# Optimization experiments

Measured on AMD Instinct MI355X. Metric: run time of the kernel, lower is better.

The kernel has to match this reference:

```python
import jax, jax.numpy as jnp
import numpy as np

# Fixed module configuration (matches init_kwargs)
B, T, H, W, C = 2, 16, 32, 32, 512
NH, DH = 8, 64          # num_heads, head_dim = C // NH
MLP = 2048
EPS = 1e-6              # flax LayerNorm default epsilon


def _xavier(key, shape):
    fan_in, fan_out = shape[-2], shape[-1]
    lim = np.sqrt(6.0 / (fan_in + fan_out)).astype(np.float32)
    return jax.random.uniform(key, shape, jnp.float32, -lim, lim)


def setup_inputs() -> dict:
    key = jax.random.key(0)
    ks = jax.random.split(key, 8)
    return {
        "x": jax.random.normal(ks[0], (B, T * H * W, C), jnp.float32),
        # per-axis (stacked: 0=time, 1=height, 2=width) attention params
        "ln_scale": jnp.ones((3, C), jnp.float32),
        "ln_bias": jnp.zeros((3, C), jnp.float32),
        "wq": _xavier(ks[1], (3, C, C)), "bq": jnp.zeros((3, C), jnp.float32),
        "wk": _xavier(ks[2], (3, C, C)), "bk": jnp.zeros((3, C), jnp.float32),
        "wv": _xavier(ks[3], (3, C, C)), "bv": jnp.zeros((3, C), jnp.float32),
        "wo": _xavier(ks[4], (3, C, C)), "bo": jnp.zeros((3, C), jnp.float32),
        # final LN + MLP params
        "ln_mlp_scale": jnp.ones((C,), jnp.float32),
        "ln_mlp_bias": jnp.zeros((C,), jnp.float32),
        "w1": _xavier(ks[5], (C, MLP)),
        "b1": jax.random.normal(ks[6], (MLP,), jnp.float32) * 1e-6,
        "w2": _xavier(ks[7], (MLP, C)),
        "b2": jnp.zeros((C,), jnp.float32),
    }


def _ln(x, scale, bias):
    m = jnp.mean(x, axis=-1, keepdims=True)
    v = jnp.var(x, axis=-1, keepdims=True)
    return (x - m) * jax.lax.rsqrt(v + EPS) * scale + bias


def _mha(x, wq, bq, wk, bk, wv, bv, wo, bo):
    # x: [Bf, S, C]; standard flax-style MHA (query scaled by 1/sqrt(head_dim))
    Bf, S, _ = x.shape
    q = (x @ wq + bq).reshape(Bf, S, NH, DH) * (1.0 / np.sqrt(DH).astype(np.float32))
    k = (x @ wk + bk).reshape(Bf, S, NH, DH)
    v = (x @ wv + bv).reshape(Bf, S, NH, DH)
    a = jax.nn.softmax(jnp.einsum('bqhd,bkhd->bhqk', q, k), axis=-1)
    o = jnp.einsum('bhqk,bkhd->bqhd', a, v).reshape(Bf, S, C)
    return o @ wo + bo


def _axial(x5, axis, sc, bi, wq, bq, wk, bk, wv, bv, wo, bo):
    # fold all non-`axis` spatial dims into batch, attend along `axis`
    other = [a for a in (1, 2, 3) if a != axis]
    perm = [0] + other + [axis, 4]
    xp = jnp.transpose(x5, perm)                      # [..., S_axis, C]
    pshape = xp.shape
    x1 = xp.reshape(-1, pshape[-2], C)                # [Bf, S_axis, C]
    y = _mha(_ln(x1, sc, bi), wq, bq, wk, bk, wv, bv, wo, bo) + x1  # pre-LN residual
    y = y.reshape(pshape)
    inv = list(np.argsort(perm))
    return jnp.transpose(y, inv)


def reference(x, ln_scale, ln_bias, wq, bq, wk, bk, wv, bv, wo, bo,
              ln_mlp_scale, ln_mlp_bias, w1, b1, w2, b2):
    x5 = x.reshape(B, T, H, W, C)
    for i, axis in enumerate((1, 2, 3)):  # time, height, width
        x5 = _axial(x5, axis, ln_scale[i], ln_bias[i], wq[i], bq[i],
                    wk[i], bk[i], wv[i], bv[i], wo[i], bo[i])
    xf = x5.reshape(B, T * H * W, C)
    y = _ln(xf, ln_mlp_scale, ln_mlp_bias)
    y = jax.nn.gelu(y @ w1 + b1) @ w2 + b2            # gelu approximate=True (flax default)
    return xf + y
```

## Files before the change

kernel.cpp:

```cpp
#include <hip/hip_runtime.h>
#include <hip/hip_bf16.h>

typedef __attribute__((ext_vector_type(8))) short short8;
typedef __attribute__((ext_vector_type(4))) float f32x4;

static __device__ __forceinline__ short f2bf(float f) {
    union { __hip_bfloat16 h; short s; } u;
    u.h = __float2bfloat16(f);
    return u.s;
}

static __device__ __forceinline__ float gelu_tanh(float v) {
    const float c = 0.7978845608028654f;
    float t = tanhf(c * (v + 0.044715f * v * v * v));
    return 0.5f * v * (1.f + t);
}

static __device__ __forceinline__ void gload16(const void* g, void* l) {
    __builtin_amdgcn_global_load_lds(
        (const __attribute__((address_space(1))) void*)g,
        (__attribute__((address_space(3))) void*)l, 16, 0, 0);
}

__global__ __launch_bounds__(256) void cvt_weights(
    const float* __restrict__ wq, const float* __restrict__ wk,
    const float* __restrict__ wv, const float* __restrict__ wo,
    const float* __restrict__ w1, const float* __restrict__ w2,
    short* __restrict__ wT)
{
    const long NSQ = 12L * 262144;
    long gid = (long)blockIdx.x * 256 + threadIdx.x;
    if (gid < NSQ) {
        int m = (int)(gid >> 18);
        int rem = (int)(gid & 262143);
        int n = rem >> 9, k = rem & 511;
        int a = m >> 2, t = m & 3;
        const float* src = (t == 0) ? wq : (t == 1) ? wk : (t == 2) ? wv : wo;
        wT[gid] = f2bf(src[(long)a * 262144 + (long)k * 512 + n]);
    } else if (gid < NSQ + 1048576) {
        int r = (int)(gid - NSQ);
        int n = r >> 9, k = r & 511;
        wT[gid] = f2bf(w1[(long)k * 2048 + n]);
    } else {
        int r = (int)(gid - NSQ - 1048576);
        int n = r >> 11, k = r & 2047;
        wT[gid] = f2bf(w2[(long)k * 512 + n]);
    }
}

__global__ __launch_bounds__(256) void ln_kernel(
    const float* __restrict__ x, const float* __restrict__ sc,
    const float* __restrict__ bi, short* __restrict__ out)
{
    int row = blockIdx.x * 4 + (threadIdx.x >> 6);
    int lane = threadIdx.x & 63;
    const float* xr = x + (long)row * 512 + lane * 8;
    f32x4 v0 = *(const f32x4*)xr;
    f32x4 v1 = *(const f32x4*)(xr + 4);
    float s = 0.f, ss = 0.f;
#pragma unroll
    for (int i = 0; i < 4; i++) { s += v0[i] + v1[i]; ss += v0[i] * v0[i] + v1[i] * v1[i]; }
#pragma unroll
    for (int m = 1; m < 64; m <<= 1) { s += __shfl_xor(s, m, 64); ss += __shfl_xor(ss, m, 64); }
    float mean = s * (1.f / 512.f);
    float var  = ss * (1.f / 512.f) - mean * mean;
    float rs = rsqrtf(var + 1e-6f);
    f32x4 s0 = *(const f32x4*)(sc + lane * 8);
    f32x4 s1 = *(const f32x4*)(sc + lane * 8 + 4);
    f32x4 b0 = *(const f32x4*)(bi + lane * 8);
    f32x4 b1 = *(const f32x4*)(bi + lane * 8 + 4);
    short8 o;
#pragma unroll
    for (int i = 0; i < 4; i++) o[i]     = f2bf((v0[i] - mean) * rs * s0[i] + b0[i]);
#pragma unroll
    for (int i = 0; i < 4; i++) o[4 + i] = f2bf((v1[i] - mean) * rs * s1[i] + b1[i]);
    *(short8*)(out + (long)row * 512 + lane * 8) = o;
}

template<int EPI>
__global__ __launch_bounds__(256, 2) void gemm_nt(
    const short* __restrict__ A, const short* __restrict__ Bt,
    const float* __restrict__ bias, const float* __restrict__ bias2,
    const float* __restrict__ bias3,
    const float* __restrict__ res, float* __restrict__ outf,
    short* __restrict__ outb, int M, int N, int K, float scale)
{
    __shared__ __align__(16) short As[128 * 64];
    __shared__ __align__(16) short Bs[128 * 64];
    const int t = threadIdx.x;
    const int lane = t & 63, wid = t >> 6;
    const int wm = wid >> 1, wn = wid & 1;
    const int m0 = blockIdx.x * 128, n0 = blockIdx.y * 128;

    const short* Ag = A  + (long)m0 * K;
    const short* Bg = Bt + (long)n0 * K;

    f32x4 acc[4][4];
#pragma unroll
    for (int i = 0; i < 4; i++)
#pragma unroll
        for (int j = 0; j < 4; j++) acc[i][j] = (f32x4){0.f, 0.f, 0.f, 0.f};

    const long rowOff = (long)(t >> 3) * K + (t & 7) * 8;
    const int  ldsOff = t * 16;
    const int NT = K >> 6;

    for (int tt = 0; tt < NT; ++tt) {
        const short* Asrc = Ag + tt * 64 + rowOff;
        const short* Bsrc = Bg + tt * 64 + rowOff;
#pragma unroll
        for (int c = 0; c < 4; c++) {
            gload16(Asrc + (long)c * 32 * K, (char*)As + c * 4096 + ldsOff);
            gload16(Bsrc + (long)c * 32 * K, (char*)Bs + c * 4096 + ldsOff);
        }
        __syncthreads();

        const int arow = wm * 64 + (lane & 15);
        const int brow = wn * 64 + (lane & 15);
        const int kb = (lane >> 4) * 16;
#pragma unroll
        for (int ks = 0; ks < 2; ++ks) {
            short8 af[4], bfr[4];
#pragma unroll
            for (int f = 0; f < 4; f++) {
                af[f]  = *(short8*)((char*)As + (arow + f * 16) * 128 + kb + ks * 64);
                bfr[f] = *(short8*)((char*)Bs + (brow + f * 16) * 128 + kb + ks * 64);
            }
#pragma unroll
            for (int i = 0; i < 4; i++)
#pragma unroll
                for (int j = 0; j < 4; j++)
                    acc[i][j] = __builtin_amdgcn_mfma_f32_16x16x32_bf16(af[i], bfr[j], acc[i][j], 0, 0, 0);
        }
        __syncthreads();
    }

    if (EPI == 1) {
#pragma unroll
        for (int j = 0; j < 4; j++) {
            int col = n0 + wn * 64 + j * 16 + (lane & 15);
            float bv = bias[col];
#pragma unroll
            for (int i = 0; i < 4; i++) {
                int row0 = m0 + wm * 64 + i * 16 + ((lane >> 4) << 2);
#pragma unroll
                for (int r = 0; r < 4; r++) {
                    long idx = (long)(row0 + r) * N + col;
                    outf[idx] = acc[i][j][r] + bv + res[idx];
                }
            }
        }
    } else {
        float* sl = (float*)(wid < 2 ? (void*)As : (void*)Bs) + (wid & 1) * 2048;
        const int r0g = m0 + wm * 64;
        const int c0g = n0 + wn * 64;
#pragma unroll
        for (int half = 0; half < 2; ++half) {
#pragma unroll
            for (int jj = 0; jj < 2; ++jj) {
                int j = half * 2 + jj;
                int col = c0g + j * 16 + (lane & 15);
                float bv, sc_part = 1.f;
                if (EPI == 3) {
                    int part = col >> 9;
                    const float* bp = (part == 0) ? bias : (part == 1) ? bias2 : bias3;
                    bv = bp[col & 511];
                    if (part == 0) sc_part = scale;
                } else {
                    bv = bias[col];
                }
#pragma unroll
                for (int i = 0; i < 4; i++)
#pragma unroll
                    for (int r = 0; r < 4; r++) {
                        int rl = i * 16 + ((lane >> 4) << 2) + r;
                        int cl = jj * 16 + (lane & 15);
                        float v = (acc[i][j][r] + bv) * sc_part;
                        if (EPI == 2) v = gelu_tanh(v);
                        sl[(rl * 32 + cl) ^ ((rl & 7) << 2)] = v;
                    }
            }
            __syncthreads();
#pragma unroll
            for (int s = 0; s < 4; s++) {
                int rl = s * 16 + (lane >> 2);
                int fb = rl * 32 + (lane & 3) * 8;
                int sw = (rl & 7) << 2;
                f32x4 lo = *(f32x4*)&sl[fb ^ sw];
                f32x4 hi = *(f32x4*)&sl[(fb + 4) ^ sw];
                short8 o;
#pragma unroll
                for (int e = 0; e < 4; e++) { o[e] = f2bf(lo[e]); o[4 + e] = f2bf(hi[e]); }
                *(short8*)(outb + (long)(r0g + rl) * N + c0g + half * 32 + (lane & 3) * 8) = o;
            }
            if (half == 0) __syncthreads();
        }
    }
}

template<int S, int PASS>
__global__ __launch_bounds__(64) void attn_kernel(
    const short* __restrict__ Q, const short* __restrict__ Kx,
    const short* __restrict__ V, short* __restrict__ O, int ld)
{
    constexpr int MF = S / 16;
    constexpr int SP = 32;
    __shared__ __align__(16) short P_lds[S * SP];
    __shared__ __align__(16) short Vt[64 * SP];

    const int lane = threadIdx.x;
    const int pair = blockIdx.x;
    const int head = pair & 7;
    const int bf = pair >> 3;
    long base; int stride;
    if (PASS == 0)      { base = (long)(bf >> 10) * 16384 + (bf & 1023); stride = 1024; }
    else if (PASS == 1) { int b = bf >> 9, t = (bf >> 5) & 15, w = bf & 31; base = (long)b * 16384 + t * 1024 + w; stride = 32; }
    else                { int b = bf >> 9, t = (bf >> 5) & 15, h = bf & 31; base = (long)b * 16384 + t * 1024 + (h << 5); stride = 1; }
    const int hoff = head * 64;

    if (S == 16) {
        short8 z = {0, 0, 0, 0, 0, 0, 0, 0};
        *(short8*)(P_lds + lane * 8) = z;
#pragma unroll
        for (int i = 0; i < 4; i++) *(short8*)(Vt + lane * 32 + i * 8) = z;
        __syncthreads();
    }

    short8 qf[MF][2], kf[MF][2];
#pragma unroll
    for (int f = 0; f < MF; f++) {
        int r = f * 16 + (lane & 15);
        const short* qp = Q + (base + (long)r * stride) * ld + hoff + ((lane >> 4) * 8);
        qf[f][0] = *(const short8*)qp;
        qf[f][1] = *(const short8*)(qp + 32);
        const short* kp = Kx + (base + (long)r * stride) * ld + hoff + ((lane >> 4) * 8);
        kf[f][0] = *(const short8*)kp;
        kf[f][1] = *(const short8*)(kp + 32);
    }

    short8 vv[4];
    const int vr  = (S == 32) ? (lane & 31) : (lane & 15);
    const int vd0 = (S == 32) ? ((lane >> 5) * 32) : ((lane >> 4) * 16);
    constexpr int NVC = (S == 32) ? 4 : 2;
    {
        const short* vp = V + (base + (long)vr * stride) * ld + hoff + vd0;
#pragma unroll
        for (int c = 0; c < NVC; c++) vv[c] = *(const short8*)(vp + c * 8);
    }
#pragma unroll
    for (int c = 0; c < NVC; c++)
#pragma unroll
        for (int e = 0; e < 8; e++)
            Vt[(vd0 + c * 8 + e) * SP + vr] = vv[c][e];

    f32x4 zero4 = {0.f, 0.f, 0.f, 0.f};
    f32x4 sc[MF][MF];
#pragma unroll
    for (int i = 0; i < MF; i++)
#pragma unroll
        for (int j = 0; j < MF; j++) {
            f32x4 a = __builtin_amdgcn_mfma_f32_16x16x32_bf16(qf[i][0], kf[j][0], zero4, 0, 0, 0);
            sc[i][j] = __builtin_amdgcn_mfma_f32_16x16x32_bf16(qf[i][1], kf[j][1], a, 0, 0, 0);
        }

#pragma unroll
    for (int i = 0; i < MF; i++) {
#pragma unroll
        for (int r = 0; r < 4; r++) {
            float mx = sc[i][0][r];
            if (MF == 2) mx = fmaxf(mx, sc[i][1][r]);
#pragma unroll
            for (int m = 1; m < 16; m <<= 1) mx = fmaxf(mx, __shfl_xor(mx, m, 64));
            float e0 = expf(sc[i][0][r] - mx);
            float e1 = (MF == 2) ? expf(sc[i][1][r] - mx) : 0.f;
            float sum = e0 + e1;
#pragma unroll
            for (int m = 1; m < 16; m <<= 1) sum += __shfl_xor(sum, m, 64);
            float inv = 1.f / sum;
            int row = i * 16 + ((lane >> 4) << 2) + r;
            P_lds[row * SP + (lane & 15)] = f2bf(e0 * inv);
            if (MF == 2) P_lds[row * SP + 16 + (lane & 15)] = f2bf(e1 * inv);
        }
    }
    __syncthreads();

    short8 pa[MF];
#pragma unroll
    for (int f = 0; f < MF; f++)
        pa[f] = *(const short8*)(P_lds + (f * 16 + (lane & 15)) * SP + (lane >> 4) * 8);
    short8 vbf[4];
#pragma unroll
    for (int n = 0; n < 4; n++)
        vbf[n] = *(const short8*)(Vt + (n * 16 + (lane & 15)) * SP + (lane >> 4) * 8);
    f32x4 of[MF][4];
#pragma unroll
    for (int f = 0; f < MF; f++)
#pragma unroll
        for (int n = 0; n < 4; n++)
            of[f][n] = __builtin_amdgcn_mfma_f32_16x16x32_bf16(pa[f], vbf[n], zero4, 0, 0, 0);

#pragma unroll
    for (int f = 0; f < MF; f++) {
        int q0 = f * 16 + ((lane >> 4) << 2);
#pragma unroll
        for (int n = 0; n < 4; n++) {
            int d = n * 16 + (lane & 15);
#pragma unroll
            for (int r = 0; r < 4; r++)
                O[(base + (long)(q0 + r) * stride) * 512 + hoff + d] = f2bf(of[f][n][r]);
        }
    }
}

extern "C" void kernel_launch(void* const* d_in, const int* in_sizes, int n_in,
                              void* d_out, int out_size, void* d_ws, size_t ws_size,
                              hipStream_t stream)
{
    const float* x   = (const float*)d_in[0];
    const float* lns = (const float*)d_in[1];
    const float* lnb = (const float*)d_in[2];
    const float* wq  = (const float*)d_in[3];
    const float* bq  = (const float*)d_in[4];
    const float* wk  = (const float*)d_in[5];
    const float* bk  = (const float*)d_in[6];
    const float* wv  = (const float*)d_in[7];
    const float* bv  = (const float*)d_in[8];
    const float* wo  = (const float*)d_in[9];
    const float* bo  = (const float*)d_in[10];
    const float* lms = (const float*)d_in[11];
    const float* lmb = (const float*)d_in[12];
    const float* w1  = (const float*)d_in[13];
    const float* b1  = (const float*)d_in[14];
    const float* w2  = (const float*)d_in[15];
    const float* b2  = (const float*)d_in[16];

    char* ws = (char*)d_ws;
    short* wT   = (short*)ws;
    short* bufA = (short*)(ws + 10485760);
    short* big  = (short*)(ws + 10485760 + 33554432);
    float* xcur = (float*)d_out;

    const int M = 32768;

    cvt_weights<<<20480, 256, 0, stream>>>(wq, wk, wv, wo, w1, w2, wT);

    for (int p = 0; p < 3; ++p) {
        const float* xin = (p == 0) ? x : xcur;
        ln_kernel<<<8192, 256, 0, stream>>>(xin, lns + p * 512, lnb + p * 512, bufA);
        const short* wqkvT = wT + (long)(p * 4) * 262144;
        const short* woT   = wT + (long)(p * 4 + 3) * 262144;
        gemm_nt<3><<<dim3(256, 12), 256, 0, stream>>>(bufA, wqkvT,
            bq + p * 512, bk + p * 512, bv + p * 512,
            nullptr, nullptr, big, M, 1536, 512, 0.125f);
        const short* qb = big, *kb = big + 512, *vbp = big + 1024;
        if (p == 0)      attn_kernel<16, 0><<<16384, 64, 0, stream>>>(qb, kb, vbp, bufA, 1536);
        else if (p == 1) attn_kernel<32, 1><<<8192, 64, 0, stream>>>(qb, kb, vbp, bufA, 1536);
        else             attn_kernel<32, 2><<<8192, 64, 0, stream>>>(qb, kb, vbp, bufA, 1536);
        gemm_nt<1><<<dim3(256, 4), 256, 0, stream>>>(bufA, woT,
            bo + p * 512, nullptr, nullptr, xin, xcur, nullptr, M, 512, 512, 1.f);
    }

    ln_kernel<<<8192, 256, 0, stream>>>(xcur, lms, lmb, bufA);
    const short* w1T = wT + 12L * 262144;
    const short* w2T = wT + 12L * 262144 + 1048576;
    gemm_nt<2><<<dim3(256, 16), 256, 0, stream>>>(bufA, w1T, b1,
        nullptr, nullptr, nullptr, nullptr, big, M, 2048, 512, 1.f);
    gemm_nt<1><<<dim3(256, 4), 256, 0, stream>>>(big, w2T, b2,
        nullptr, nullptr, xcur, xcur, nullptr, M, 512, 2048, 1.f);
}
```

Measured before the change: 1.103 ms.

## Register-prefetch next GEMM tile and XOR-swizzle LDS layout

```diff
diff --git a/kernel.cpp b/kernel.cpp
--- a/kernel.cpp
+++ b/kernel.cpp
@@ -14,12 +14,6 @@
     const float c = 0.7978845608028654f;
     float t = tanhf(c * (v + 0.044715f * v * v * v));
     return 0.5f * v * (1.f + t);
-}
-
-static __device__ __forceinline__ void gload16(const void* g, void* l) {
-    __builtin_amdgcn_global_load_lds(
-        (const __attribute__((address_space(1))) void*)g,
-        (__attribute__((address_space(3))) void*)l, 16, 0, 0);
 }
 
 __global__ __launch_bounds__(256) void cvt_weights(
@@ -101,20 +95,33 @@
 #pragma unroll
         for (int j = 0; j < 4; j++) acc[i][j] = (f32x4){0.f, 0.f, 0.f, 0.f};
 
-    const long rowOff = (long)(t >> 3) * K + (t & 7) * 8;
-    const int  ldsOff = t * 16;
+    short8 areg[4], breg[4];
+#pragma unroll
+    for (int c = 0; c < 4; c++) {
+        int g = c * 256 + t; int r = g >> 3, kc = g & 7;
+        areg[c] = *(const short8*)(Ag + (long)r * K + kc * 8);
+        breg[c] = *(const short8*)(Bg + (long)r * K + kc * 8);
+    }
     const int NT = K >> 6;
-
     for (int tt = 0; tt < NT; ++tt) {
-        const short* Asrc = Ag + tt * 64 + rowOff;
-        const short* Bsrc = Bg + tt * 64 + rowOff;
 #pragma unroll
         for (int c = 0; c < 4; c++) {
-            gload16(Asrc + (long)c * 32 * K, (char*)As + c * 4096 + ldsOff);
-            gload16(Bsrc + (long)c * 32 * K, (char*)Bs + c * 4096 + ldsOff);
+            int g = c * 256 + t; int r = g >> 3, kc = g & 7;
+            int off = r * 128 + ((kc * 16) ^ ((r & 7) << 4));
+            *(short8*)((char*)As + off) = areg[c];
+            *(short8*)((char*)Bs + off) = breg[c];
+        }
+        if (tt + 1 < NT) {
+            const short* Ag2 = Ag + (tt + 1) * 64;
+            const short* Bg2 = Bg + (tt + 1) * 64;
+#pragma unroll
+            for (int c = 0; c < 4; c++) {
+                int g = c * 256 + t; int r = g >> 3, kc = g & 7;
+                areg[c] = *(const short8*)(Ag2 + (long)r * K + kc * 8);
+                breg[c] = *(const short8*)(Bg2 + (long)r * K + kc * 8);
+            }
         }
         __syncthreads();
-
         const int arow = wm * 64 + (lane & 15);
         const int brow = wn * 64 + (lane & 15);
         const int kb = (lane >> 4) * 16;
@@ -123,8 +130,10 @@
             short8 af[4], bfr[4];
 #pragma unroll
             for (int f = 0; f < 4; f++) {
-                af[f]  = *(short8*)((char*)As + (arow + f * 16) * 128 + kb + ks * 64);
-                bfr[f] = *(short8*)((char*)Bs + (brow + f * 16) * 128 + kb + ks * 64);
+                int ra = arow + f * 16;
+                af[f]  = *(short8*)((char*)As + ra * 128 + ((kb + ks * 64) ^ ((ra & 7) << 4)));
+                int rb = brow + f * 16;
+                bfr[f] = *(short8*)((char*)Bs + rb * 128 + ((kb + ks * 64) ^ ((rb & 7) << 4)));
             }
 #pragma unroll
             for (int i = 0; i < 4; i++)
```

New measurement: 904.6 us. -18.0%, faster.

## Double-buffer GEMM LDS tiles to overlap global loads with MFMA compute

Applied to the files above, without the earlier changes.

```diff
diff --git a/kernel.cpp b/kernel.cpp
--- a/kernel.cpp
+++ b/kernel.cpp
@@ -85,8 +85,7 @@
     const float* __restrict__ res, float* __restrict__ outf,
     short* __restrict__ outb, int M, int N, int K, float scale)
 {
-    __shared__ __align__(16) short As[128 * 64];
-    __shared__ __align__(16) short Bs[128 * 64];
+    __shared__ __align__(16) short AB[2][2][8192];
     const int t = threadIdx.x;
     const int lane = t & 63, wid = t >> 6;
     const int wm = wid >> 1, wn = wid & 1;
@@ -103,18 +102,33 @@
 
     const long rowOff = (long)(t >> 3) * K + (t & 7) * 8;
     const int  ldsOff = t * 16;
+    char* const lbase = (char*)AB;
     const int NT = K >> 6;
 
+#pragma unroll
+    for (int c = 0; c < 4; c++) {
+        gload16(Ag + rowOff + (long)c * 32 * K, lbase + c * 4096 + ldsOff);
+        gload16(Bg + rowOff + (long)c * 32 * K, lbase + 16384 + c * 4096 + ldsOff);
+    }
+
+    int cur = 0;
     for (int tt = 0; tt < NT; ++tt) {
-        const short* Asrc = Ag + tt * 64 + rowOff;
-        const short* Bsrc = Bg + tt * 64 + rowOff;
-#pragma unroll
-        for (int c = 0; c < 4; c++) {
-            gload16(Asrc + (long)c * 32 * K, (char*)As + c * 4096 + ldsOff);
-            gload16(Bsrc + (long)c * 32 * K, (char*)Bs + c * 4096 + ldsOff);
-        }
-        __syncthreads();
-
+        if (tt + 1 < NT) {
+            const short* Asrc = Ag + (tt + 1) * 64 + rowOff;
+            const short* Bsrc = Bg + (tt + 1) * 64 + rowOff;
+            char* dst = lbase + (cur ^ 1) * 32768;
+#pragma unroll
+            for (int c = 0; c < 4; c++) {
+                gload16(Asrc + (long)c * 32 * K, dst + c * 4096 + ldsOff);
+                gload16(Bsrc + (long)c * 32 * K, dst + 16384 + c * 4096 + ldsOff);
+            }
+            asm volatile("s_waitcnt vmcnt(8)" ::: "memory");
+        } else {
+            asm volatile("s_waitcnt vmcnt(0)" ::: "memory");
+        }
+        asm volatile("s_barrier" ::: "memory");
+
+        const char* rb = lbase + cur * 32768;
         const int arow = wm * 64 + (lane & 15);
         const int brow = wn * 64 + (lane & 15);
         const int kb = (lane >> 4) * 16;
@@ -123,8 +137,8 @@
             short8 af[4], bfr[4];
 #pragma unroll
             for (int f = 0; f < 4; f++) {
-                af[f]  = *(short8*)((char*)As + (arow + f * 16) * 128 + kb + ks * 64);
-                bfr[f] = *(short8*)((char*)Bs + (brow + f * 16) * 128 + kb + ks * 64);
+                af[f]  = *(short8*)(rb + (arow + f * 16) * 128 + kb + ks * 64);
+                bfr[f] = *(short8*)(rb + 16384 + (brow + f * 16) * 128 + kb + ks * 64);
             }
 #pragma unroll
             for (int i = 0; i < 4; i++)
@@ -132,7 +146,8 @@
                 for (int j = 0; j < 4; j++)
                     acc[i][j] = __builtin_amdgcn_mfma_f32_16x16x32_bf16(af[i], bfr[j], acc[i][j], 0, 0, 0);
         }
-        __syncthreads();
+        asm volatile("s_barrier" ::: "memory");
+        cur ^= 1;
     }
 
     if (EPI == 1) {
@@ -151,7 +166,7 @@
             }
         }
     } else {
-        float* sl = (float*)(wid < 2 ? (void*)As : (void*)Bs) + (wid & 1) * 2048;
+        float* sl = (float*)((char*)AB + (wid >> 1) * 32768 + (wid & 1) * 8192);
         const int r0g = m0 + wm * 64;
         const int c0g = n0 + wn * 64;
 #pragma unroll
```

After: 971.5 us. 1.14x faster.
